# Optimization experiments

Measured on AMD Instinct MI355X. Metric: run time of the kernel, lower is better.

## Reference

```python
import math
import jax, jax.numpy as jnp
import numpy as np

C = 256          # channels
HID = 64         # max(int(C*0.25),16)
RH = 64          # max(C//4,32) router hidden
N, S, H, W = 8, 64, 16, 16
LOW_FREQ_RATIO = 0.2
ROUTER_TEMP = 1.0
LN_EPS = 1e-5

def gelu(v):
    return jax.nn.gelu(v, approximate=False)

def bn1d(v, s, b):  # folded eval-mode BatchNorm1d: (N,C,S)
    return v * s[None, :, None] + b[None, :, None]

def conv1x1(v, w, b=None):  # v:(N,Cin,S), w:(Cout,Cin)
    o = jnp.einsum('oc,ncs->nos', w, v)
    if b is not None:
        o = o + b[None, :, None]
    return o

def convk(v, w):  # v:(N,Cin,S), w:(Cout,Cin,K), 'same' padding
    k = w.shape[-1]
    return jax.lax.conv_general_dilated(v, w, (1,), [(k // 2, k // 2)],
                                        dimension_numbers=('NCH', 'OIH', 'NCH'))

def setup_inputs():
    key = jax.random.key(0)
    ks = iter(jax.random.split(key, 64))
    def nrm(shape, sc=0.02):
        return jax.random.normal(next(ks), shape, jnp.float32) * sc
    d = {}
    d['x'] = jax.random.normal(next(ks), (N, C, S, H, W), jnp.float32)
    d['ln_g'] = jnp.ones((C,), jnp.float32)
    d['ln_b'] = jnp.zeros((C,), jnp.float32)
    for k in (3, 5, 7):
        d['mb_w%d' % k] = nrm((C, 3 * C, k))
        d['mb_s%d' % k] = 1.0 + nrm((C,))
        d['mb_b%d' % k] = nrm((C,))
    d['mf_w'] = nrm((C, C)); d['mf_s'] = 1.0 + nrm((C,)); d['mf_b'] = nrm((C,))
    d['pg_w1'] = nrm((HID, 3)); d['pg_s1'] = 1.0 + nrm((HID,)); d['pg_b1'] = nrm((HID,))
    d['pg_w2'] = nrm((C, HID)); d['pg_b2'] = nrm((C,))
    d['pp_w'] = nrm((C, C)); d['pp_s'] = 1.0 + nrm((C,)); d['pp_b'] = nrm((C,))
    d['mg_w'] = nrm((C, 2 * C)); d['mg_b'] = nrm((C,))
    d['mo_w1'] = nrm((C, 3 * C)); d['mo_s1'] = 1.0 + nrm((C,)); d['mo_b1'] = nrm((C,))
    d['mo_w2'] = nrm((C, C))
    d['rt_w1'] = nrm((RH, C + 5)); d['rt_b1'] = nrm((RH,))
    d['rt_w2'] = nrm((3, RH)); d['rt_b2'] = nrm((3,))
    d['bp_w1'] = nrm((C, 4 * C)); d['bp_s1'] = 1.0 + nrm((C,)); d['bp_b1'] = nrm((C,))
    d['bp_w2'] = nrm((C, C))
    d['res_scale'] = jnp.full((1, C, 1), 0.05, jnp.float32)
    d['fg_w'] = nrm((C, C)); d['fg_b'] = nrm((C,))
    d['sg_w'] = nrm((C, C)); d['sg_s'] = 1.0 + nrm((C,)); d['sg_b'] = nrm((C,))
    return d

def _forward(x, ln_g, ln_b, mb_w3, mb_s3, mb_b3, mb_w5, mb_s5, mb_b5,
             mb_w7, mb_s7, mb_b7, mf_w, mf_s, mf_b,
             pg_w1, pg_s1, pg_b1, pg_w2, pg_b2, pp_w, pp_s, pp_b,
             mg_w, mg_b, mo_w1, mo_s1, mo_b1, mo_w2,
             rt_w1, rt_b1, rt_w2, rt_b2, bp_w1, bp_s1, bp_b1, bp_w2,
             res_scale, fg_w, fg_b, sg_w, sg_s, sg_b):
    n, c, s = x.shape[:3]
    x32 = x.astype(jnp.float32)
    desc = x32.mean(axis=(-1, -2))                     # (N,C,S)
    t = desc.transpose(0, 2, 1)                        # (N,S,C)
    mu = t.mean(-1, keepdims=True)
    var = t.var(-1, keepdims=True)
    dn = (((t - mu) / jnp.sqrt(var + LN_EPS)) * ln_g + ln_b).transpose(0, 2, 1)  # (N,C,S)

    def tdiff(v, order):
        dd = v[:, :, order:] - v[:, :, :-order]
        return jnp.pad(dd, ((0, 0), (0, 0), (order, 0)))
    diff1 = tdiff(dn, 1)
    diff2 = tdiff(dn, 2)

    # motion branch (multi-kernel conv1d + BN + GELU)
    mi = jnp.concatenate([dn, diff1, diff2], axis=1)   # (N,3C,S)
    motion = 0.0
    for w, bs, bb in ((mb_w3, mb_s3, mb_b3), (mb_w5, mb_s5, mb_b5), (mb_w7, mb_s7, mb_b7)):
        motion = motion + gelu(bn1d(convk(mi, w), bs, bb))
    motion = gelu(bn1d(conv1x1(motion / 3.0, mf_w), mf_s, mf_b))

    # FFT-based cycle / phase estimation
    tokens = dn.transpose(0, 2, 1)                     # (N,S,C)
    freq = jnp.fft.rfft(tokens, axis=1, norm='ortho')  # (N,F,C) complex
    fe = jnp.abs(freq).mean(-1)                        # (N,F)
    Fb = fe.shape[1]
    low = min(max(int(round(Fb * LOW_FREQ_RATIO)), 1), Fb - 1)
    he = fe[:, low:]
    peak_rel = jnp.argmax(he, axis=-1)                 # (N,)
    peak_idx = peak_rel + low
    peak_val = jnp.take_along_axis(he, peak_rel[:, None], axis=1)
    cycle_conf = peak_val / jnp.maximum(he.sum(axis=1, keepdims=True), 1e-6)  # (N,1)
    peak_norm = peak_idx.astype(jnp.float32)[:, None] / float(Fb - 1)
    mean_freq = freq.mean(-1)                          # (N,F) complex
    dom = jnp.take_along_axis(mean_freq, peak_idx[:, None], axis=1)[:, 0]
    dom_phase = jnp.arctan2(dom.imag, dom.real)
    tax = jnp.arange(s, dtype=jnp.float32)
    ang = (2.0 * math.pi / max(s, 1)) * peak_idx.astype(jnp.float32)
    arg = ang[:, None] * tax[None, :] + dom_phase[:, None]
    phase_cos = jnp.cos(arg)[:, None, :]               # (N,1,S)
    phase_sin = jnp.sin(arg)[:, None, :]

    cycle_token = jnp.broadcast_to(cycle_conf[:, :, None], (n, 1, s))
    pf = jnp.concatenate([phase_cos, phase_sin, cycle_token], axis=1)  # (N,3,S)
    pgate = jax.nn.sigmoid(conv1x1(gelu(bn1d(conv1x1(pf, pg_w1), pg_s1, pg_b1)), pg_w2, pg_b2))
    phase = gelu(bn1d(conv1x1(dn * pgate, pp_w), pp_s, pp_b))

    # bidirectional EMA memory via lax.scan
    gate = jax.nn.sigmoid(conv1x1(jnp.concatenate([dn, jnp.abs(diff1)], axis=1), mg_w, mg_b))
    g = gate.transpose(2, 0, 1)                        # (S,N,C)
    dd = dn.transpose(2, 0, 1)
    def step(st, gd):
        gt, dt = gd
        st = gt * st + (1.0 - gt) * dt
        return st, st
    _, fo = jax.lax.scan(step, dd[0], (g[1:], dd[1:]))
    fwd_mem = jnp.concatenate([dd[:1], fo], axis=0).transpose(1, 2, 0)
    _, bo = jax.lax.scan(step, dd[-1], (g[-2::-1], dd[-2::-1]))
    bwd_mem = jnp.concatenate([dd[-1:], bo], axis=0)[::-1].transpose(1, 2, 0)
    memory = conv1x1(gelu(bn1d(conv1x1(
        jnp.concatenate([dn, fwd_mem, bwd_mem], axis=1), mo_w1), mo_s1, mo_b1)), mo_w2)

    # router
    seq_std = dn.std(axis=2).mean(axis=1, keepdims=True)
    diff_energy = jnp.abs(diff1).mean(axis=(1, 2))[:, None]
    motion_energy = jnp.abs(motion).mean(axis=(1, 2))[:, None]
    memory_energy = jnp.abs(memory - dn).mean(axis=(1, 2))[:, None]
    stats = jnp.concatenate([seq_std, diff_energy, cycle_conf, peak_norm,
                             memory_energy + motion_energy], axis=-1)
    ri = jnp.concatenate([dn.mean(-1), stats], axis=-1)  # (N,C+5)
    hdn = gelu(ri @ rt_w1.T + rt_b1)
    logits = hdn @ rt_w2.T + rt_b2
    bw = jax.nn.softmax(logits / max(ROUTER_TEMP, 1e-6), axis=-1)  # (N,3)
    fused = (bw[:, 0, None, None] * motion + bw[:, 1, None, None] * phase
             + bw[:, 2, None, None] * memory)

    delta = conv1x1(gelu(bn1d(conv1x1(
        jnp.concatenate([dn, fused, motion - phase, memory - dn], axis=1),
        bp_w1), bp_s1, bp_b1)), bp_w2)
    delta = delta * jax.nn.sigmoid(conv1x1(dn, fg_w, fg_b))
    delta = res_scale * delta
    delta = delta[:, :, :, None, None]                 # (N,C,S,1,1)

    sp = x32.mean(axis=2)                              # (N,C,H,W)
    sg_lin = jnp.einsum('oc,nchw->nohw', sg_w, sp)
    sgate = jax.nn.sigmoid(sg_lin * sg_s[None, :, None, None] + sg_b[None, :, None, None])
    delta = delta * sgate[:, :, None, :, :]            # (N,C,S,H,W)
    return x + delta.astype(x.dtype)

def reference(x, ln_g, ln_b, mb_w3, mb_s3, mb_b3, mb_w5, mb_s5, mb_b5,
              mb_w7, mb_s7, mb_b7, mf_w, mf_s, mf_b,
              pg_w1, pg_s1, pg_b1, pg_w2, pg_b2, pp_w, pp_s, pp_b,
              mg_w, mg_b, mo_w1, mo_s1, mo_b1, mo_w2,
              rt_w1, rt_b1, rt_w2, rt_b2, bp_w1, bp_s1, bp_b1, bp_w2,
              res_scale, fg_w, fg_b, sg_w, sg_s, sg_b):
    return _forward(x, ln_g, ln_b, mb_w3, mb_s3, mb_b3, mb_w5, mb_s5, mb_b5,
                    mb_w7, mb_s7, mb_b7, mf_w, mf_s, mf_b,
                    pg_w1, pg_s1, pg_b1, pg_w2, pg_b2, pp_w, pp_s, pp_b,
                    mg_w, mg_b, mo_w1, mo_s1, mo_b1, mo_w2,
                    rt_w1, rt_b1, rt_w2, rt_b2, bp_w1, bp_s1, bp_b1, bp_w2,
                    res_scale, fg_w, fg_b, sg_w, sg_s, sg_b)
```

## Files before the change

### kernel.cpp

```cpp
#include <hip/hip_runtime.h>
#include <math.h>

namespace {

constexpr int N_ = 8, C_ = 256, S_ = 64, HW_ = 256;
constexpr int NS = N_ * S_;
constexpr int NHW = N_ * HW_;

constexpr size_t O_DESC  = 0;
constexpr size_t O_DN    = 131072;
constexpr size_t O_MOT   = 393216;
constexpr size_t O_GATE  = 524288;
constexpr size_t O_MEM   = 786432;
constexpr size_t O_PHASE = 1048576;
constexpr size_t O_DELTA = 1441792;
constexpr size_t O_SCN   = 1572864;
constexpr size_t O_SPT   = 2752512;
constexpr size_t O_SGATE = 3276800;
constexpr size_t O_FE    = 3801088;
constexpr size_t O_MFRE  = 3801600;
constexpr size_t O_MFIM  = 3802112;
constexpr size_t O_BW    = 3802656;
constexpr size_t O_ATMF  = 3802688;
constexpr size_t O_ATMG  = 3868224;
constexpr size_t O_ATMO1 = 3999296;
constexpr size_t O_ATMO2 = 4195904;
constexpr size_t O_ATPP  = 4261440;
constexpr size_t O_ATBP1 = 4326976;
constexpr size_t O_ATBP2 = 4589120;
constexpr size_t O_ATFG  = 4654656;
constexpr size_t O_ATSG  = 4720192;
constexpr size_t O_WFRAG = 4785728;
constexpr size_t O_IM2   = 6850112;
constexpr size_t O_CONVC = 8226368;

typedef __attribute__((ext_vector_type(4))) float f32x4;
typedef __attribute__((ext_vector_type(8))) short s16x8;
typedef __attribute__((ext_vector_type(8))) unsigned short u16x8;

__device__ __forceinline__ float gelu_f(float v) {
  return 0.5f * v * (1.0f + erff(v * 0.70710678118654752f));
}
__device__ __forceinline__ float sigmoid_f(float v) {
  return 1.0f / (1.0f + expf(-v));
}
__device__ __forceinline__ unsigned short f2bf(float f) {
  unsigned int u = __float_as_uint(f);
  u += 0x7fffu + ((u >> 16) & 1u);
  return (unsigned short)(u >> 16);
}

__device__ __forceinline__ float block_sum256(float v, float* scratch) {
  #pragma unroll
  for (int off = 32; off; off >>= 1) v += __shfl_down(v, off, 64);
  int w = threadIdx.x >> 6;
  __syncthreads();
  if ((threadIdx.x & 63) == 0) scratch[w] = v;
  __syncthreads();
  return scratch[0] + scratch[1] + scratch[2] + scratch[3];
}

__device__ __forceinline__ void compute_pk(
    int n, const float* __restrict__ fe, const float* __restrict__ mfre,
    const float* __restrict__ mfim,
    float& conf, float& pnorm, float& dph, float& ang) {
  const float* f = fe + n * 33;
  float best = f[7]; int bidx = 0; float hs = 0.f;
  #pragma unroll
  for (int i = 0; i < 26; ++i) {
    float v = f[7 + i];
    hs += v;
    if (v > best) { best = v; bidx = i; }
  }
  int pi = bidx + 7;
  conf = best / fmaxf(hs, 1e-6f);
  pnorm = (float)pi * (1.f / 32.f);
  dph = atan2f(mfim[n * 33 + pi], mfre[n * 33 + pi]);
  ang = (6.283185307179586f / 64.f) * (float)pi;
}

__global__ __launch_bounds__(256) void weights_kernel(
    const float* __restrict__ wmf, const float* __restrict__ wmg,
    const float* __restrict__ wmo1, const float* __restrict__ wmo2,
    const float* __restrict__ wpp, const float* __restrict__ wbp1,
    const float* __restrict__ wbp2, const float* __restrict__ wfg,
    const float* __restrict__ wsg, float* __restrict__ ws,
    const float* __restrict__ w3, const float* __restrict__ w5,
    const float* __restrict__ w7, unsigned short* __restrict__ wf) {
  int bid = blockIdx.x;
  if (bid < 960) {
    __shared__ float tile[32][33];
    int xt = bid % 120, yt = bid / 120;
    const float* src; float* dst; int K;
    if      (xt < 8)   { src = wmf;  dst = ws + O_ATMF;  K = 256;  }
    else if (xt < 24)  { src = wmg;  dst = ws + O_ATMG;  K = 512;  xt -= 8;  }
    else if (xt < 48)  { src = wmo1; dst = ws + O_ATMO1; K = 768;  xt -= 24; }
    else if (xt < 56)  { src = wmo2; dst = ws + O_ATMO2; K = 256;  xt -= 48; }
    else if (xt < 64)  { src = wpp;  dst = ws + O_ATPP;  K = 256;  xt -= 56; }
    else if (xt < 96)  { src = wbp1; dst = ws + O_ATBP1; K = 1024; xt -= 64; }
    else if (xt < 104) { src = wbp2; dst = ws + O_ATBP2; K = 256;  xt -= 96; }
    else if (xt < 112) { src = wfg;  dst = ws + O_ATFG;  K = 256;  xt -= 104;}
    else               { src = wsg;  dst = ws + O_ATSG;  K = 256;  xt -= 112;}
    int tx = threadIdx.x & 31, ty = threadIdx.x >> 5;
    int c = xt * 32 + tx;
    #pragma unroll
    for (int i = 0; i < 4; ++i) {
      int r = yt * 32 + ty + i * 8;
      tile[ty + i * 8][tx] = src[(size_t)r * K + c];
    }
    __syncthreads();
    #pragma unroll
    for (int i = 0; i < 4; ++i) {
      int cc = xt * 32 + ty + i * 8;
      dst[(size_t)cc * 256 + yt * 32 + tx] = tile[tx][ty + i * 8];
    }
  } else {
    int g = (bid - 960) * 256 + threadIdx.x;
    int lane = g & 63;
    int m16 = (g >> 6) % 48;
    int kchunk = (g >> 6) / 48;
    int o = m16 * 16 + (lane & 15);
    int conv = o >> 8, oc = o & 255;
    int q = lane >> 4;
    u16x8 outv;
    #pragma unroll
    for (int j = 0; j < 8; ++j) {
      int k = kchunk * 32 + q * 8 + j;
      int ic = k / 7;
      int tau = k - ic * 7 - 3;
      float v = 0.f;
      if (conv == 0) {
        if (tau >= -1 && tau <= 1) v = w3[((size_t)oc * 768 + ic) * 3 + (tau + 1)];
      } else if (conv == 1) {
        if (tau >= -2 && tau <= 2) v = w5[((size_t)oc * 768 + ic) * 5 + (tau + 2)];
      } else {
        v = w7[((size_t)oc * 768 + ic) * 7 + (tau + 3)];
      }
      outv[j] = f2bf(v);
    }
    *((u16x8*)wf + g) = outv;
  }
}

__global__ __launch_bounds__(256) void reduce_x_kernel(
    const float* __restrict__ x, float* __restrict__ desc_t, float* __restrict__ sp_t) {
  int nc = blockIdx.x; int n = nc >> 8; int c = nc & 255;
  int t = threadIdx.x; int w = t >> 6; int l = t & 63;
  const float4* x4 = (const float4*)x + (size_t)nc * 4096;
  float4 sa = {0.f, 0.f, 0.f, 0.f};
  for (int i = 0; i < 16; ++i) {
    int s = w * 16 + i;
    float4 v = x4[(size_t)s * 64 + l];
    sa.x += v.x; sa.y += v.y; sa.z += v.z; sa.w += v.w;
    float ds = v.x + v.y + v.z + v.w;
    #pragma unroll
    for (int off = 32; off; off >>= 1) ds += __shfl_down(ds, off, 64);
    if (l == 0) desc_t[((size_t)n * 64 + s) * 256 + c] = ds * (1.f / 256.f);
  }
  __shared__ float4 lsp[4][64];
  lsp[w][l] = sa;
  __syncthreads();
  if (t < 64) {
    float4 a = lsp[0][t], b = lsp[1][t], c2 = lsp[2][t], d = lsp[3][t];
    float4 tot;
    tot.x = a.x + b.x + c2.x + d.x; tot.y = a.y + b.y + c2.y + d.y;
    tot.z = a.z + b.z + c2.z + d.z; tot.w = a.w + b.w + c2.w + d.w;
    size_t base = ((size_t)n * 256 + t * 4) * 256 + c;
    sp_t[base]       = tot.x * (1.f / 64.f);
    sp_t[base + 256] = tot.y * (1.f / 64.f);
    sp_t[base + 512] = tot.z * (1.f / 64.f);
    sp_t[base + 768] = tot.w * (1.f / 64.f);
  }
}

__global__ __launch_bounds__(256) void ln_kernel(
    const float* __restrict__ desc_t, const float* __restrict__ g,
    const float* __restrict__ b, float* __restrict__ dn_t) {
  __shared__ float sc[4];
  int col = blockIdx.x; int t = threadIdx.x;
  float v = desc_t[(size_t)col * 256 + t];
  float s1 = block_sum256(v, sc);
  float s2 = block_sum256(v * v, sc);
  float mu = s1 * (1.f / 256.f);
  float var = s2 * (1.f / 256.f) - mu * mu;
  float r = rsqrtf(var + 1e-5f);
  dn_t[(size_t)col * 256 + t] = (v - mu) * r * g[t] + b[t];
}

__global__ __launch_bounds__(256) void post_ln_kernel(
    const float* __restrict__ dn_t, const float* __restrict__ At_mg,
    const float* __restrict__ mg_b, float* __restrict__ gate_t,
    unsigned short* __restrict__ imf,
    float* __restrict__ fe, float* __restrict__ mfre, float* __restrict__ mfim) {
  __shared__ __align__(16) float smem[2048];
  int bid = blockIdx.x;
  int t = threadIdx.x;
  if (bid < 128) {
    int c0 = bid * 4;
    float4 f0, f1;
    {
      float d[4], a[4];
      #pragma unroll
      for (int i = 0; i < 4; ++i) {
        int col = c0 + i; int s = col & 63;
        float dd = dn_t[(size_t)col * 256 + t];
        float d1 = (s >= 1) ? dd - dn_t[(size_t)(col - 1) * 256 + t] : 0.f;
        d[i] = dd; a[i] = fabsf(d1);
      }
      f0.x = d[0]; f0.y = d[1]; f0.z = d[2]; f0.w = d[3];
      f1.x = a[0]; f1.y = a[1]; f1.z = a[2]; f1.w = a[3];
    }
    *(float4*)&smem[t * 4] = f0;
    *(float4*)&smem[(256 + t) * 4] = f1;
    __syncthreads();
    float a0 = 0.f, a1 = 0.f, a2 = 0.f, a3 = 0.f;
    #pragma unroll 4
    for (int k = 0; k < 512; ++k) {
      float a = At_mg[(size_t)k * 256 + t];
      float4 b = *(const float4*)&smem[k * 4];
      a0 += a * b.x; a1 += a * b.y; a2 += a * b.z; a3 += a * b.w;
    }
    float bb = mg_b[t];
    gate_t[(size_t)(c0 + 0) * 256 + t] = sigmoid_f(a0 + bb);
    gate_t[(size_t)(c0 + 1) * 256 + t] = sigmoid_f(a1 + bb);
    gate_t[(size_t)(c0 + 2) * 256 + t] = sigmoid_f(a2 + bb);
    gate_t[(size_t)(c0 + 3) * 256 + t] = sigmoid_f(a3 + bb);
  } else if (bid < 1472) {
    int g = (bid - 128) * 256 + t;
    int lane = g & 63;
    int c16 = (g >> 6) % 32;
    int kchunk = (g >> 6) / 32;
    int col = c16 * 16 + (lane & 15);
    int n = col >> 6, s = col & 63;
    int q = lane >> 4;
    const float* base = dn_t + (size_t)n * 16384;
    u16x8 outv;
    #pragma unroll
    for (int j = 0; j < 8; ++j) {
      int k = kchunk * 32 + q * 8 + j;
      int ic = k / 7;
      int tau = k - ic * 7 - 3;
      int stream = ic >> 8, c = ic & 255;
      int sp = s + tau;
      float v = 0.f;
      if (sp >= 0 && sp < 64) {
        float d = base[(size_t)sp * 256 + c];
        if (stream == 0) v = d;
        else if (stream == 1) v = (sp >= 1) ? d - base[(size_t)(sp - 1) * 256 + c] : 0.f;
        else v = (sp >= 2) ? d - base[(size_t)(sp - 2) * 256 + c] : 0.f;
      }
      outv[j] = f2bf(v);
    }
    *((u16x8*)imf + g) = outv;
  } else {
    int b = bid - 1472; int n = b / 33; int f = b % 33;
    float* cs = smem; float* sn = smem + 64; float* scr = smem + 128;
    if (t < 64) {
      int ft = (f * t) & 63;
      float ang = -6.283185307179586f * (float)ft * (1.f / 64.f);
      cs[t] = cosf(ang); sn[t] = sinf(ang);
    }
    __syncthreads();
    float re = 0.f, im = 0.f;
    const float* base = dn_t + (size_t)n * 16384 + t;
    for (int s = 0; s < 64; ++s) {
      float v = base[(size_t)s * 256];
      re += v * cs[s]; im += v * sn[s];
    }
    re *= 0.125f; im *= 0.125f;
    float mag = sqrtf(re * re + im * im);
    float sm = block_sum256(mag, scr);
    float sr = block_sum256(re, scr);
    float si = block_sum256(im, scr);
    if (t == 0) {
      fe[b]   = sm * (1.f / 256.f);
      mfre[b] = sr * (1.f / 256.f);
      mfim[b] = si * (1.f / 256.f);
    }
  }
}

__global__ __launch_bounds__(256) void conv_scan_kernel(
    const unsigned short* __restrict__ wf, const unsigned short* __restrict__ imf,
    float* __restrict__ partial,
    const float* __restrict__ dn_t, const float* __restrict__ gate_t,
    float* __restrict__ scn) {
  __shared__ float smem[16384];
  int bid = blockIdx.x;
  int t = threadIdx.x;
  if (bid < 384) {
    int mt = bid % 12; int rem = bid / 12;
    int nt = rem % 8; int kp = rem / 8;
    int lane = t & 63;
    int w = t >> 6;
    int m16 = mt * 4 + w;
    const s16x8* wfp = (const s16x8*)wf;
    const s16x8* imp = (const s16x8*)imf;
    f32x4 acc0 = {0.f,0.f,0.f,0.f}, acc1 = {0.f,0.f,0.f,0.f};
    f32x4 acc2 = {0.f,0.f,0.f,0.f}, acc3 = {0.f,0.f,0.f,0.f};
    #pragma unroll 2
    for (int cc = 0; cc < 42; ++cc) {
      int kc = kp * 42 + cc;
      s16x8 a = wfp[(size_t)(kc * 48 + m16) * 64 + lane];
      s16x8 b0 = imp[(size_t)(kc * 32 + nt * 4 + 0) * 64 + lane];
      s16x8 b1 = imp[(size_t)(kc * 32 + nt * 4 + 1) * 64 + lane];
      s16x8 b2 = imp[(size_t)(kc * 32 + nt * 4 + 2) * 64 + lane];
      s16x8 b3 = imp[(size_t)(kc * 32 + nt * 4 + 3) * 64 + lane];
      acc0 = __builtin_amdgcn_mfma_f32_16x16x32_bf16(a, b0, acc0, 0, 0, 0);
      acc1 = __builtin_amdgcn_mfma_f32_16x16x32_bf16(a, b1, acc1, 0, 0, 0);
      acc2 = __builtin_amdgcn_mfma_f32_16x16x32_bf16(a, b2, acc2, 0, 0, 0);
      acc3 = __builtin_amdgcn_mfma_f32_16x16x32_bf16(a, b3, acc3, 0, 0, 0);
    }
    int q = lane >> 4, ln = lane & 15;
    int o0 = m16 * 16 + q * 4;
    float* pb = partial + (size_t)kp * 393216;
    #pragma unroll
    for (int r = 0; r < 4; ++r) {
      size_t row = (size_t)(o0 + r) * 512;
      pb[row + (nt * 4 + 0) * 16 + ln] = acc0[r];
      pb[row + (nt * 4 + 1) * 16 + ln] = acc1[r];
      pb[row + (nt * 4 + 2) * 16 + ln] = acc2[r];
      pb[row + (nt * 4 + 3) * 16 + ln] = acc3[r];
    }
  } else {
    int idx = bid - 384;
    int n = idx >> 1, half = idx & 1;
    float* ld = smem;
    float* lg = smem + 8192;
    const float* dsrc = dn_t + (size_t)n * 16384 + half * 128;
    const float* gsrc = gate_t + (size_t)n * 16384 + half * 128;
    for (int i = t; i < 8192; i += 256) {
      int s = i >> 7, j = i & 127;
      ld[i] = dsrc[(size_t)s * 256 + j];
      lg[i] = gsrc[(size_t)s * 256 + j];
    }
    __syncthreads();
    int cl = t & 127;
    int c = half * 128 + cl;
    size_t ob = (size_t)n * 64 * 512 + c;
    if (t < 128) {
      float st = ld[cl];
      scn[ob] = st;
      for (int s = 1; s < 64; ++s) {
        float g = lg[s * 128 + cl], d = ld[s * 128 + cl];
        st = g * st + (1.f - g) * d;
        scn[ob + (size_t)s * 512] = st;
      }
    } else {
      float st = ld[63 * 128 + cl];
      scn[ob + (size_t)63 * 512 + 256] = st;
      for (int s = 62; s >= 0; --s) {
        float g = lg[s * 128 + cl], d = ld[s * 128 + cl];
        st = g * st + (1.f - g) * d;
        scn[ob + (size_t)s * 512 + 256] = st;
      }
    }
  }
}

__global__ __launch_bounds__(256) void mid_kernel(
    const float* __restrict__ P,
    const float* __restrict__ s3, const float* __restrict__ b3,
    const float* __restrict__ s5, const float* __restrict__ b5,
    const float* __restrict__ s7, const float* __restrict__ b7,
    const float* __restrict__ At_mf, const float* __restrict__ mf_s,
    const float* __restrict__ mf_b, float* __restrict__ motion_t,
    const float* __restrict__ dn_t, const float* __restrict__ scn,
    const float* __restrict__ At1, const float* __restrict__ sc1, const float* __restrict__ bi1,
    const float* __restrict__ At2, float* __restrict__ mem_t,
    const float* __restrict__ fe, const float* __restrict__ mfre, const float* __restrict__ mfim,
    const float* __restrict__ pg_w1, const float* __restrict__ pg_s1, const float* __restrict__ pg_b1,
    const float* __restrict__ pg_w2, const float* __restrict__ pg_b2,
    const float* __restrict__ At_pp, const float* __restrict__ pp_s, const float* __restrict__ pp_b,
    float* __restrict__ phase_t,
    const float* __restrict__ At_sg, const float* __restrict__ sp_t,
    const float* __restrict__ sg_s, const float* __restrict__ sg_b,
    float* __restrict__ sgate_t) {
  __shared__ __align__(16) float smem[4096];
  int bid = blockIdx.x;
  int t = threadIdx.x;
  if (bid < 128) {
    int c0 = bid * 4;
    float4 v3 = {0,0,0,0}, v5 = {0,0,0,0}, v7 = {0,0,0,0};
    #pragma unroll
    for (int kp = 0; kp < 4; ++kp) {
      const float* base = P + (size_t)kp * 393216 + c0;
      float4 x3 = *(const float4*)(base + (size_t)t * 512);
      float4 x5 = *(const float4*)(base + (size_t)(t + 256) * 512);
      float4 x7 = *(const float4*)(base + (size_t)(t + 512) * 512);
      v3.x += x3.x; v3.y += x3.y; v3.z += x3.z; v3.w += x3.w;
      v5.x += x5.x; v5.y += x5.y; v5.z += x5.z; v5.w += x5.w;
      v7.x += x7.x; v7.y += x7.y; v7.z += x7.z; v7.w += x7.w;
    }
    float s3v = s3[t], b3v = b3[t], s5v = s5[t], b5v = b5[t], s7v = s7[t], b7v = b7[t];
    float4 ms;
    ms.x = (gelu_f(v3.x*s3v+b3v) + gelu_f(v5.x*s5v+b5v) + gelu_f(v7.x*s7v+b7v)) * (1.f/3.f);
    ms.y = (gelu_f(v3.y*s3v+b3v) + gelu_f(v5.y*s5v+b5v) + gelu_f(v7.y*s7v+b7v)) * (1.f/3.f);
    ms.z = (gelu_f(v3.z*s3v+b3v) + gelu_f(v5.z*s5v+b5v) + gelu_f(v7.z*s7v+b7v)) * (1.f/3.f);
    ms.w = (gelu_f(v3.w*s3v+b3v) + gelu_f(v5.w*s5v+b5v) + gelu_f(v7.w*s7v+b7v)) * (1.f/3.f);
    *(float4*)&smem[t * 4] = ms;
    __syncthreads();
    float a0 = 0.f, a1 = 0.f, a2 = 0.f, a3 = 0.f;
    #pragma unroll 4
    for (int k = 0; k < 256; ++k) {
      float a = At_mf[(size_t)k * 256 + t];
      float4 b = *(const float4*)&smem[k * 4];
      a0 += a * b.x; a1 += a * b.y; a2 += a * b.z; a3 += a * b.w;
    }
    float sv = mf_s[t], bv2 = mf_b[t];
    motion_t[(size_t)(c0 + 0) * 256 + t] = gelu_f(a0 * sv + bv2);
    motion_t[(size_t)(c0 + 1) * 256 + t] = gelu_f(a1 * sv + bv2);
    motion_t[(size_t)(c0 + 2) * 256 + t] = gelu_f(a2 * sv + bv2);
    motion_t[(size_t)(c0 + 3) * 256 + t] = gelu_f(a3 * sv + bv2);
  } else if (bid < 256) {
    int c0 = (bid - 128) * 4;
    float* bv = smem;
    float* h4 = smem + 3072;
    float4 r0, r1, r2;
    #pragma unroll
    for (int i = 0; i < 4; ++i) {
      int col = c0 + i;
      ((float*)&r0)[i] = dn_t[(size_t)col * 256 + t];
      ((float*)&r1)[i] = scn[(size_t)col * 512 + t];
      ((float*)&r2)[i] = scn[(size_t)col * 512 + 256 + t];
    }
    *(float4*)&bv[t * 4] = r0;
    *(float4*)&bv[(256 + t) * 4] = r1;
    *(float4*)&bv[(512 + t) * 4] = r2;
    __syncthreads();
    float a0 = 0.f, a1 = 0.f, a2 = 0.f, a3 = 0.f;
    #pragma unroll 4
    for (int k = 0; k < 768; ++k) {
      float a = At1[(size_t)k * 256 + t];
      float4 b = *(const float4*)&bv[k * 4];
      a0 += a * b.x; a1 += a * b.y; a2 += a * b.z; a3 += a * b.w;
    }
    float sv = sc1[t], bb = bi1[t];
    float4 h;
    h.x = gelu_f(a0 * sv + bb); h.y = gelu_f(a1 * sv + bb);
    h.z = gelu_f(a2 * sv + bb); h.w = gelu_f(a3 * sv + bb);
    *(float4*)&h4[t * 4] = h;
    __syncthreads();
    float c0a = 0.f, c1a = 0.f, c2a = 0.f, c3a = 0.f;
    #pragma unroll 4
    for (int k = 0; k < 256; ++k) {
      float a = At2[(size_t)k * 256 + t];
      float4 b = *(const float4*)&h4[k * 4];
      c0a += a * b.x; c1a += a * b.y; c2a += a * b.z; c3a += a * b.w;
    }
    mem_t[(size_t)(c0 + 0) * 256 + t] = c0a;
    mem_t[(size_t)(c0 + 1) * 256 + t] = c1a;
    mem_t[(size_t)(c0 + 2) * 256 + t] = c2a;
    mem_t[(size_t)(c0 + 3) * 256 + t] = c3a;
  } else if (bid < 384) {
    int c0 = (bid - 256) * 4; int n = c0 >> 6; int s0 = c0 & 63;
    float* hh4 = smem;
    float* pin4 = smem + 256;
    float conf, pnorm, dph, ang;
    compute_pk(n, fe, mfre, mfim, conf, pnorm, dph, ang);
    (void)pnorm;
    if (t < 64) {
      float w0 = pg_w1[t * 3 + 0], w1 = pg_w1[t * 3 + 1], w2 = pg_w1[t * 3 + 2];
      float sv = pg_s1[t], bb = pg_b1[t];
      float4 hv;
      #pragma unroll
      for (int i = 0; i < 4; ++i) {
        float arg = ang * (float)(s0 + i) + dph;
        float v = w0 * cosf(arg) + w1 * sinf(arg) + w2 * conf;
        ((float*)&hv)[i] = gelu_f(v * sv + bb);
      }
      *(float4*)&hh4[t * 4] = hv;
    }
    __syncthreads();
    float p0, p1, p2, p3;
    {
      float bb = pg_b2[t];
      float a0 = bb, a1 = bb, a2 = bb, a3 = bb;
      const float* wrow = pg_w2 + t * 64;
      #pragma unroll 8
      for (int j = 0; j < 64; ++j) {
        float w = wrow[j];
        float4 h = *(const float4*)&hh4[j * 4];
        a0 += w * h.x; a1 += w * h.y; a2 += w * h.z; a3 += w * h.w;
      }
      p0 = sigmoid_f(a0); p1 = sigmoid_f(a1); p2 = sigmoid_f(a2); p3 = sigmoid_f(a3);
    }
    float4 pin;
    pin.x = dn_t[(size_t)(c0 + 0) * 256 + t] * p0;
    pin.y = dn_t[(size_t)(c0 + 1) * 256 + t] * p1;
    pin.z = dn_t[(size_t)(c0 + 2) * 256 + t] * p2;
    pin.w = dn_t[(size_t)(c0 + 3) * 256 + t] * p3;
    *(float4*)&pin4[t * 4] = pin;
    __syncthreads();
    float a0 = 0.f, a1 = 0.f, a2 = 0.f, a3 = 0.f;
    #pragma unroll 4
    for (int k = 0; k < 256; ++k) {
      float a = At_pp[(size_t)k * 256 + t];
      float4 b = *(const float4*)&pin4[k * 4];
      a0 += a * b.x; a1 += a * b.y; a2 += a * b.z; a3 += a * b.w;
    }
    float sv = pp_s[t], bb = pp_b[t];
    phase_t[(size_t)(c0 + 0) * 256 + t] = gelu_f(a0 * sv + bb);
    phase_t[(size_t)(c0 + 1) * 256 + t] = gelu_f(a1 * sv + bb);
    phase_t[(size_t)(c0 + 2) * 256 + t] = gelu_f(a2 * sv + bb);
    phase_t[(size_t)(c0 + 3) * 256 + t] = gelu_f(a3 * sv + bb);
  } else {
    int c0 = (bid - 384) * 4;
    float4 r0;
    #pragma unroll
    for (int i = 0; i < 4; ++i) {
      ((float*)&r0)[i] = sp_t[(size_t)(c0 + i) * 256 + t];
    }
    *(float4*)&smem[t * 4] = r0;
    __syncthreads();
    float a0 = 0.f, a1 = 0.f, a2 = 0.f, a3 = 0.f;
    #pragma unroll 4
    for (int k = 0; k < 256; ++k) {
      float a = At_sg[(size_t)k * 256 + t];
      float4 b = *(const float4*)&smem[k * 4];
      a0 += a * b.x; a1 += a * b.y; a2 += a * b.z; a3 += a * b.w;
    }
    float sv = sg_s[t], bb = sg_b[t];
    sgate_t[(size_t)(c0 + 0) * 256 + t] = sigmoid_f(a0 * sv + bb);
    sgate_t[(size_t)(c0 + 1) * 256 + t] = sigmoid_f(a1 * sv + bb);
    sgate_t[(size_t)(c0 + 2) * 256 + t] = sigmoid_f(a2 * sv + bb);
    sgate_t[(size_t)(c0 + 3) * 256 + t] = sigmoid_f(a3 * sv + bb);
  }
}

__global__ __launch_bounds__(256) void router_kernel(
    const float* __restrict__ dn_t, const float* __restrict__ motion_t,
    const float* __restrict__ memory_t,
    const float* __restrict__ fe, const float* __restrict__ mfre,
    const float* __restrict__ mfim,
    const float* __restrict__ rt_w1, const float* __restrict__ rt_b1,
    const float* __restrict__ rt_w2, const float* __restrict__ rt_b2,
    float* __restrict__ bw) {
  int n = blockIdx.x; int c = threadIdx.x;
  __shared__ float ri[261];
  __shared__ float h2[64];
  __shared__ float lg[3];
  __shared__ float sc[4];
  float sum = 0.f, sq = 0.f, ad1 = 0.f, amot = 0.f, amem = 0.f, prev = 0.f;
  for (int s = 0; s < 64; ++s) {
    size_t i = ((size_t)n * 64 + s) * 256 + c;
    float d = dn_t[i];
    sum += d; sq += d * d;
    if (s > 0) ad1 += fabsf(d - prev);
    prev = d;
    amot += fabsf(motion_t[i]);
    amem += fabsf(memory_t[i] - d);
  }
  float mean = sum * (1.f / 64.f);
  float var = sq * (1.f / 64.f) - mean * mean;
  float stdc = sqrtf(fmaxf(var, 0.f));
  ri[c] = mean;
  float rstd = block_sum256(stdc, sc);
  float rad1 = block_sum256(ad1, sc);
  float rmot = block_sum256(amot, sc);
  float rmem = block_sum256(amem, sc);
  if (c == 0) {
    float conf, pnorm, dph, ang;
    compute_pk(n, fe, mfre, mfim, conf, pnorm, dph, ang);
    (void)dph; (void)ang;
    ri[256] = rstd * (1.f / 256.f);
    ri[257] = rad1 * (1.f / 16384.f);
    ri[258] = conf;
    ri[259] = pnorm;
    ri[260] = (rmem + rmot) * (1.f / 16384.f);
  }
  __syncthreads();
  if (c < 64) {
    float acc = rt_b1[c];
    const float* wrow = rt_w1 + c * 261;
    for (int i = 0; i < 261; ++i) acc += wrow[i] * ri[i];
    h2[c] = gelu_f(acc);
  }
  __syncthreads();
  if (c < 3) {
    float acc = rt_b2[c];
    const float* wrow = rt_w2 + c * 64;
    #pragma unroll 8
    for (int j = 0; j < 64; ++j) acc += wrow[j] * h2[j];
    lg[c] = acc;
  }
  __syncthreads();
  if (c == 0) {
    float m = fmaxf(lg[0], fmaxf(lg[1], lg[2]));
    float e0 = expf(lg[0] - m), e1 = expf(lg[1] - m), e2 = expf(lg[2] - m);
    float inv = 1.f / (e0 + e1 + e2);
    bw[n * 3 + 0] = e0 * inv; bw[n * 3 + 1] = e1 * inv; bw[n * 3 + 2] = e2 * inv;
  }
}

__global__ __launch_bounds__(256) void delta_kernel(
    const float* __restrict__ dn_t, const float* __restrict__ motion_t,
    const float* __restrict__ phase_t, const float* __restrict__ mem_t,
    const float* __restrict__ bw,
    const float* __restrict__ At_fg, const float* __restrict__ fg_b,
    const float* __restrict__ At1, const float* __restrict__ sc1, const float* __restrict__ bi1,
    const float* __restrict__ At2, const float* __restrict__ rs,
    float* __restrict__ delta_t) {
  __shared__ __align__(16) float bv[1024];
  __shared__ __align__(16) float4 part[4][64];
  __shared__ float hs[256];
  __shared__ float fgs[256];
  int col = blockIdx.x; int n = col >> 6; int t = threadIdx.x;
  int w = t >> 6, ln = t & 63;
  int oq = t >> 2, oc = t & 3;
  float w0 = bw[n * 3 + 0], w1 = bw[n * 3 + 1], w2 = bw[n * 3 + 2];
  size_t idx = (size_t)col * 256 + t;
  float d = dn_t[idx], m = motion_t[idx], p = phase_t[idx], me = mem_t[idx];
  bv[t]       = d;
  bv[256 + t] = w0 * m + w1 * p + w2 * me;
  bv[512 + t] = m - p;
  bv[768 + t] = me - d;
  __syncthreads();
  {
    float a0 = 0.f, a1 = 0.f, a2 = 0.f, a3 = 0.f;
    int k0 = w * 64;
    #pragma unroll 4
    for (int k = k0; k < k0 + 64; ++k) {
      float b = bv[k];
      float4 a = *(const float4*)(At_fg + (size_t)k * 256 + ln * 4);
      a0 += a.x * b; a1 += a.y * b; a2 += a.z * b; a3 += a.w * b;
    }
    float4 pr; pr.x = a0; pr.y = a1; pr.z = a2; pr.w = a3;
    part[w][ln] = pr;
  }
  __syncthreads();
  {
    float r = ((const float*)&part[0][oq])[oc] + ((const float*)&part[1][oq])[oc]
            + ((const float*)&part[2][oq])[oc] + ((const float*)&part[3][oq])[oc];
    fgs[t] = sigmoid_f(r + fg_b[t]);
  }
  __syncthreads();
  {
    float a0 = 0.f, a1 = 0.f, a2 = 0.f, a3 = 0.f;
    int k0 = w * 256;
    #pragma unroll 4
    for (int k = k0; k < k0 + 256; ++k) {
      float b = bv[k];
      float4 a = *(const float4*)(At1 + (size_t)k * 256 + ln * 4);
      a0 += a.x * b; a1 += a.y * b; a2 += a.z * b; a3 += a.w * b;
    }
    float4 pr; pr.x = a0; pr.y = a1; pr.z = a2; pr.w = a3;
    part[w][ln] = pr;
  }
  __syncthreads();
  {
    float r = ((const float*)&part[0][oq])[oc] + ((const float*)&part[1][oq])[oc]
            + ((const float*)&part[2][oq])[oc] + ((const float*)&part[3][oq])[oc];
    hs[t] = gelu_f(r * sc1[t] + bi1[t]);
  }
  __syncthreads();
  {
    float a0 = 0.f, a1 = 0.f, a2 = 0.f, a3 = 0.f;
    int k0 = w * 64;
    #pragma unroll 4
    for (int k = k0; k < k0 + 64; ++k) {
      float b = hs[k];
      float4 a = *(const float4*)(At2 + (size_t)k * 256 + ln * 4);
      a0 += a.x * b; a1 += a.y * b; a2 += a.z * b; a3 += a.w * b;
    }
    float4 pr; pr.x = a0; pr.y = a1; pr.z = a2; pr.w = a3;
    part[w][ln] = pr;
  }
  __syncthreads();
  {
    float r = ((const float*)&part[0][oq])[oc] + ((const float*)&part[1][oq])[oc]
            + ((const float*)&part[2][oq])[oc] + ((const float*)&part[3][oq])[oc];
    delta_t[idx] = r * fgs[t] * rs[t];
  }
}

__global__ __launch_bounds__(256) void final_kernel(
    const float* __restrict__ x, const float* __restrict__ delta_t,
    const float* __restrict__ sgate_t, float* __restrict__ out) {
  int nc = blockIdx.x; int n = nc >> 8; int c = nc & 255;
  int t = threadIdx.x;
  __shared__ float dlt[64];
  __shared__ float4 sgs4[64];
  if (t < 64) dlt[t] = delta_t[((size_t)n * 64 + t) * 256 + c];
  ((float*)sgs4)[t] = sgate_t[((size_t)n * 256 + t) * 256 + c];
  __syncthreads();
  const float4* x4 = (const float4*)x + (size_t)nc * 4096;
  float4* o4 = (float4*)out + (size_t)nc * 4096;
  int w = t >> 6, l = t & 63;
  float4 sg = sgs4[l];
  for (int i = 0; i < 16; ++i) {
    int s = w * 16 + i;
    float d = dlt[s];
    float4 v = x4[(size_t)s * 64 + l];
    v.x += d * sg.x; v.y += d * sg.y; v.z += d * sg.z; v.w += d * sg.w;
    o4[(size_t)s * 64 + l] = v;
  }
}

}

extern "C" void kernel_launch(void* const* d_in, const int* in_sizes, int n_in,
                              void* d_out, int out_size, void* d_ws, size_t ws_size,
                              hipStream_t stream) {
  const float* x      = (const float*)d_in[0];
  const float* ln_g   = (const float*)d_in[1];
  const float* ln_b   = (const float*)d_in[2];
  const float* mb_w3  = (const float*)d_in[3];
  const float* mb_s3  = (const float*)d_in[4];
  const float* mb_b3  = (const float*)d_in[5];
  const float* mb_w5  = (const float*)d_in[6];
  const float* mb_s5  = (const float*)d_in[7];
  const float* mb_b5  = (const float*)d_in[8];
  const float* mb_w7  = (const float*)d_in[9];
  const float* mb_s7  = (const float*)d_in[10];
  const float* mb_b7  = (const float*)d_in[11];
  const float* mf_w   = (const float*)d_in[12];
  const float* mf_s   = (const float*)d_in[13];
  const float* mf_b   = (const float*)d_in[14];
  const float* pg_w1  = (const float*)d_in[15];
  const float* pg_s1  = (const float*)d_in[16];
  const float* pg_b1  = (const float*)d_in[17];
  const float* pg_w2  = (const float*)d_in[18];
  const float* pg_b2  = (const float*)d_in[19];
  const float* pp_w   = (const float*)d_in[20];
  const float* pp_s   = (const float*)d_in[21];
  const float* pp_b   = (const float*)d_in[22];
  const float* mg_w   = (const float*)d_in[23];
  const float* mg_b   = (const float*)d_in[24];
  const float* mo_w1  = (const float*)d_in[25];
  const float* mo_s1  = (const float*)d_in[26];
  const float* mo_b1  = (const float*)d_in[27];
  const float* mo_w2  = (const float*)d_in[28];
  const float* rt_w1  = (const float*)d_in[29];
  const float* rt_b1  = (const float*)d_in[30];
  const float* rt_w2  = (const float*)d_in[31];
  const float* rt_b2  = (const float*)d_in[32];
  const float* bp_w1  = (const float*)d_in[33];
  const float* bp_s1  = (const float*)d_in[34];
  const float* bp_b1  = (const float*)d_in[35];
  const float* bp_w2  = (const float*)d_in[36];
  const float* res_sc = (const float*)d_in[37];
  const float* fg_w   = (const float*)d_in[38];
  const float* fg_b   = (const float*)d_in[39];
  const float* sg_w   = (const float*)d_in[40];
  const float* sg_s   = (const float*)d_in[41];
  const float* sg_b   = (const float*)d_in[42];
  float* ws = (float*)d_ws;
  float* out = (float*)d_out;
  unsigned short* wfrag = (unsigned short*)(ws + O_WFRAG);
  unsigned short* im2   = (unsigned short*)(ws + O_IM2);

  weights_kernel<<<2976, 256, 0, stream>>>(mf_w, mg_w, mo_w1, mo_w2, pp_w, bp_w1,
      bp_w2, fg_w, sg_w, ws, mb_w3, mb_w5, mb_w7, wfrag);
  reduce_x_kernel<<<2048, 256, 0, stream>>>(x, ws + O_DESC, ws + O_SPT);
  ln_kernel<<<512, 256, 0, stream>>>(ws + O_DESC, ln_g, ln_b, ws + O_DN);
  post_ln_kernel<<<1736, 256, 0, stream>>>(ws + O_DN, ws + O_ATMG, mg_b, ws + O_GATE,
      im2, ws + O_FE, ws + O_MFRE, ws + O_MFIM);
  conv_scan_kernel<<<400, 256, 0, stream>>>(wfrag, im2, ws + O_CONVC,
      ws + O_DN, ws + O_GATE, ws + O_SCN);
  mid_kernel<<<896, 256, 0, stream>>>(ws + O_CONVC, mb_s3, mb_b3, mb_s5, mb_b5,
      mb_s7, mb_b7, ws + O_ATMF, mf_s, mf_b, ws + O_MOT,
      ws + O_DN, ws + O_SCN, ws + O_ATMO1, mo_s1, mo_b1, ws + O_ATMO2, ws + O_MEM,
      ws + O_FE, ws + O_MFRE, ws + O_MFIM,
      pg_w1, pg_s1, pg_b1, pg_w2, pg_b2, ws + O_ATPP, pp_s, pp_b, ws + O_PHASE,
      ws + O_ATSG, ws + O_SPT, sg_s, sg_b, ws + O_SGATE);
  router_kernel<<<8, 256, 0, stream>>>(ws + O_DN, ws + O_MOT, ws + O_MEM,
      ws + O_FE, ws + O_MFRE, ws + O_MFIM, rt_w1, rt_b1, rt_w2, rt_b2, ws + O_BW);
  delta_kernel<<<512, 256, 0, stream>>>(ws + O_DN, ws + O_MOT, ws + O_PHASE, ws + O_MEM,
      ws + O_BW, ws + O_ATFG, fg_b, ws + O_ATBP1, bp_s1, bp_b1, ws + O_ATBP2, res_sc,
      ws + O_DELTA);
  final_kernel<<<2048, 256, 0, stream>>>(x, ws + O_DELTA, ws + O_SGATE, out);
}
```

Before: 564.4 us.

## Merge weight prep with x reduction, fuse spatial gate into final kernel

Combines the weight-transpose/fragment kernel and the x reduction kernel into one launch, removing a launch and letting the two independent workloads overlap. The spatial gate GEMV moves out of mid_kernel into final_kernel, where each block computes its own 256 sigmoid gates from sp_t and a sg_w row, so the sgate intermediate buffer is gone. The bidirectional scan now uses 4 blocks per batch instead of 2 for more parallelism. The cost is extra per-block GEMV work in final_kernel, which repeats reads of sp_t across channels.

```diff
diff --git a/kernel.cpp b/kernel.cpp
--- a/kernel.cpp
+++ b/kernel.cpp
@@ -16,7 +16,6 @@
 constexpr size_t O_DELTA = 1441792;
 constexpr size_t O_SCN   = 1572864;
 constexpr size_t O_SPT   = 2752512;
-constexpr size_t O_SGATE = 3276800;
 constexpr size_t O_FE    = 3801088;
 constexpr size_t O_MFRE  = 3801600;
 constexpr size_t O_MFIM  = 3802112;
@@ -29,7 +28,6 @@
 constexpr size_t O_ATBP1 = 4326976;
 constexpr size_t O_ATBP2 = 4589120;
 constexpr size_t O_ATFG  = 4654656;
-constexpr size_t O_ATSG  = 4720192;
 constexpr size_t O_WFRAG = 4785728;
 constexpr size_t O_IM2   = 6850112;
 constexpr size_t O_CONVC = 8226368;
@@ -79,18 +77,49 @@
   ang = (6.283185307179586f / 64.f) * (float)pi;
 }
 
-__global__ __launch_bounds__(256) void weights_kernel(
+__global__ __launch_bounds__(256) void reduce_weights_kernel(
+    const float* __restrict__ x, float* __restrict__ desc_t, float* __restrict__ sp_t,
     const float* __restrict__ wmf, const float* __restrict__ wmg,
     const float* __restrict__ wmo1, const float* __restrict__ wmo2,
     const float* __restrict__ wpp, const float* __restrict__ wbp1,
     const float* __restrict__ wbp2, const float* __restrict__ wfg,
-    const float* __restrict__ wsg, float* __restrict__ ws,
+    float* __restrict__ ws,
     const float* __restrict__ w3, const float* __restrict__ w5,
     const float* __restrict__ w7, unsigned short* __restrict__ wf) {
   int bid = blockIdx.x;
-  if (bid < 960) {
+  int t = threadIdx.x;
+  if (bid < 2048) {
+    int nc = bid; int n = nc >> 8; int c = nc & 255;
+    int w = t >> 6; int l = t & 63;
+    const float4* x4 = (const float4*)x + (size_t)nc * 4096;
+    float4 sa = {0.f, 0.f, 0.f, 0.f};
+    for (int i = 0; i < 16; ++i) {
+      int s = w * 16 + i;
+      float4 v = x4[(size_t)s * 64 + l];
+      sa.x += v.x; sa.y += v.y; sa.z += v.z; sa.w += v.w;
+      float ds = v.x + v.y + v.z + v.w;
+      #pragma unroll
+      for (int off = 32; off; off >>= 1) ds += __shfl_down(ds, off, 64);
+      if (l == 0) desc_t[((size_t)n * 64 + s) * 256 + c] = ds * (1.f / 256.f);
+    }
+    __shared__ float4 lsp[4][64];
+    lsp[w][l] = sa;
+    __syncthreads();
+    if (t < 64) {
+      float4 a = lsp[0][t], b = lsp[1][t], c2 = lsp[2][t], d = lsp[3][t];
+      float4 tot;
+      tot.x = a.x + b.x + c2.x + d.x; tot.y = a.y + b.y + c2.y + d.y;
+      tot.z = a.z + b.z + c2.z + d.z; tot.w = a.w + b.w + c2.w + d.w;
+      size_t base = ((size_t)n * 256 + t * 4) * 256 + c;
+      sp_t[base]       = tot.x * (1.f / 64.f);
+      sp_t[base + 256] = tot.y * (1.f / 64.f);
+      sp_t[base + 512] = tot.z * (1.f / 64.f);
+      sp_t[base + 768] = tot.w * (1.f / 64.f);
+    }
+  } else if (bid < 2048 + 896) {
     __shared__ float tile[32][33];
-    int xt = bid % 120, yt = bid / 120;
+    int b2 = bid - 2048;
+    int xt = b2 % 112, yt = b2 / 112;
     const float* src; float* dst; int K;
     if      (xt < 8)   { src = wmf;  dst = ws + O_ATMF;  K = 256;  }
     else if (xt < 24)  { src = wmg;  dst = ws + O_ATMG;  K = 512;  xt -= 8;  }
@@ -99,9 +128,8 @@
     else if (xt < 64)  { src = wpp;  dst = ws + O_ATPP;  K = 256;  xt -= 56; }
     else if (xt < 96)  { src = wbp1; dst = ws + O_ATBP1; K = 1024; xt -= 64; }
     else if (xt < 104) { src = wbp2; dst = ws + O_ATBP2; K = 256;  xt -= 96; }
-    else if (xt < 112) { src = wfg;  dst = ws + O_ATFG;  K = 256;  xt -= 104;}
-    else               { src = wsg;  dst = ws + O_ATSG;  K = 256;  xt -= 112;}
-    int tx = threadIdx.x & 31, ty = threadIdx.x >> 5;
+    else               { src = wfg;  dst = ws + O_ATFG;  K = 256;  xt -= 104;}
+    int tx = t & 31, ty = t >> 5;
     int c = xt * 32 + tx;
     #pragma unroll
     for (int i = 0; i < 4; ++i) {
@@ -115,7 +143,7 @@
       dst[(size_t)cc * 256 + yt * 32 + tx] = tile[tx][ty + i * 8];
     }
   } else {
-    int g = (bid - 960) * 256 + threadIdx.x;
+    int g = (bid - 2048 - 896) * 256 + t;
     int lane = g & 63;
     int m16 = (g >> 6) % 48;
     int kchunk = (g >> 6) / 48;
@@ -139,37 +167,6 @@
       outv[j] = f2bf(v);
     }
     *((u16x8*)wf + g) = outv;
-  }
-}
-
-__global__ __launch_bounds__(256) void reduce_x_kernel(
-    const float* __restrict__ x, float* __restrict__ desc_t, float* __restrict__ sp_t) {
-  int nc = blockIdx.x; int n = nc >> 8; int c = nc & 255;
-  int t = threadIdx.x; int w = t >> 6; int l = t & 63;
-  const float4* x4 = (const float4*)x + (size_t)nc * 4096;
-  float4 sa = {0.f, 0.f, 0.f, 0.f};
-  for (int i = 0; i < 16; ++i) {
-    int s = w * 16 + i;
-    float4 v = x4[(size_t)s * 64 + l];
-    sa.x += v.x; sa.y += v.y; sa.z += v.z; sa.w += v.w;
-    float ds = v.x + v.y + v.z + v.w;
-    #pragma unroll
-    for (int off = 32; off; off >>= 1) ds += __shfl_down(ds, off, 64);
-    if (l == 0) desc_t[((size_t)n * 64 + s) * 256 + c] = ds * (1.f / 256.f);
-  }
-  __shared__ float4 lsp[4][64];
-  lsp[w][l] = sa;
-  __syncthreads();
-  if (t < 64) {
-    float4 a = lsp[0][t], b = lsp[1][t], c2 = lsp[2][t], d = lsp[3][t];
-    float4 tot;
-    tot.x = a.x + b.x + c2.x + d.x; tot.y = a.y + b.y + c2.y + d.y;
-    tot.z = a.z + b.z + c2.z + d.z; tot.w = a.w + b.w + c2.w + d.w;
-    size_t base = ((size_t)n * 256 + t * 4) * 256 + c;
-    sp_t[base]       = tot.x * (1.f / 64.f);
-    sp_t[base + 256] = tot.y * (1.f / 64.f);
-    sp_t[base + 512] = tot.z * (1.f / 64.f);
-    sp_t[base + 768] = tot.w * (1.f / 64.f);
   }
 }
 
@@ -285,7 +282,7 @@
     float* __restrict__ partial,
     const float* __restrict__ dn_t, const float* __restrict__ gate_t,
     float* __restrict__ scn) {
-  __shared__ float smem[16384];
+  __shared__ float smem[8192];
   int bid = blockIdx.x;
   int t = threadIdx.x;
   if (bid < 384) {
@@ -324,33 +321,33 @@
     }
   } else {
     int idx = bid - 384;
-    int n = idx >> 1, half = idx & 1;
+    int n = idx >> 2, qr = idx & 3;
     float* ld = smem;
-    float* lg = smem + 8192;
-    const float* dsrc = dn_t + (size_t)n * 16384 + half * 128;
-    const float* gsrc = gate_t + (size_t)n * 16384 + half * 128;
-    for (int i = t; i < 8192; i += 256) {
-      int s = i >> 7, j = i & 127;
+    float* lg = smem + 4096;
+    const float* dsrc = dn_t + (size_t)n * 16384 + qr * 64;
+    const float* gsrc = gate_t + (size_t)n * 16384 + qr * 64;
+    for (int i = t; i < 4096; i += 256) {
+      int s = i >> 6, j = i & 63;
       ld[i] = dsrc[(size_t)s * 256 + j];
       lg[i] = gsrc[(size_t)s * 256 + j];
     }
     __syncthreads();
-    int cl = t & 127;
-    int c = half * 128 + cl;
+    int cl = t & 63;
+    int c = qr * 64 + cl;
     size_t ob = (size_t)n * 64 * 512 + c;
-    if (t < 128) {
+    if (t < 64) {
       float st = ld[cl];
       scn[ob] = st;
       for (int s = 1; s < 64; ++s) {
-        float g = lg[s * 128 + cl], d = ld[s * 128 + cl];
+        float g = lg[s * 64 + cl], d = ld[s * 64 + cl];
         st = g * st + (1.f - g) * d;
         scn[ob + (size_t)s * 512] = st;
       }
-    } else {
-      float st = ld[63 * 128 + cl];
+    } else if (t < 128) {
+      float st = ld[63 * 64 + cl];
       scn[ob + (size_t)63 * 512 + 256] = st;
       for (int s = 62; s >= 0; --s) {
-        float g = lg[s * 128 + cl], d = ld[s * 128 + cl];
+        float g = lg[s * 64 + cl], d = ld[s * 64 + cl];
         st = g * st + (1.f - g) * d;
         scn[ob + (size_t)s * 512 + 256] = st;
       }
@@ -372,10 +369,7 @@
     const float* __restrict__ pg_w1, const float* __restrict__ pg_s1, const float* __restrict__ pg_b1,
     const float* __restrict__ pg_w2, const float* __restrict__ pg_b2,
     const float* __restrict__ At_pp, const float* __restrict__ pp_s, const float* __restrict__ pp_b,
-    float* __restrict__ phase_t,
-    const float* __restrict__ At_sg, const float* __restrict__ sp_t,
-    const float* __restrict__ sg_s, const float* __restrict__ sg_b,
-    float* __restrict__ sgate_t) {
+    float* __restrict__ phase_t) {
   __shared__ __align__(16) float smem[4096];
   int bid = blockIdx.x;
   int t = threadIdx.x;
@@ -452,7 +446,7 @@
     mem_t[(size_t)(c0 + 1) * 256 + t] = c1a;
     mem_t[(size_t)(c0 + 2) * 256 + t] = c2a;
     mem_t[(size_t)(c0 + 3) * 256 + t] = c3a;
-  } else if (bid < 384) {
+  } else {
     int c0 = (bid - 256) * 4; int n = c0 >> 6; int s0 = c0 & 63;
     float* hh4 = smem;
     float* pin4 = smem + 256;
@@ -504,27 +498,6 @@
     phase_t[(size_t)(c0 + 1) * 256 + t] = gelu_f(a1 * sv + bb);
     phase_t[(size_t)(c0 + 2) * 256 + t] = gelu_f(a2 * sv + bb);
     phase_t[(size_t)(c0 + 3) * 256 + t] = gelu_f(a3 * sv + bb);
-  } else {
-    int c0 = (bid - 384) * 4;
-    float4 r0;
-    #pragma unroll
-    for (int i = 0; i < 4; ++i) {
-      ((float*)&r0)[i] = sp_t[(size_t)(c0 + i) * 256 + t];
-    }
-    *(float4*)&smem[t * 4] = r0;
-    __syncthreads();
-    float a0 = 0.f, a1 = 0.f, a2 = 0.f, a3 = 0.f;
-    #pragma unroll 4
-    for (int k = 0; k < 256; ++k) {
-      float a = At_sg[(size_t)k * 256 + t];
-      float4 b = *(const float4*)&smem[k * 4];
-      a0 += a * b.x; a1 += a * b.y; a2 += a * b.z; a3 += a * b.w;
-    }
-    float sv = sg_s[t], bb = sg_b[t];
-    sgate_t[(size_t)(c0 + 0) * 256 + t] = sigmoid_f(a0 * sv + bb);
-    sgate_t[(size_t)(c0 + 1) * 256 + t] = sigmoid_f(a1 * sv + bb);
-    sgate_t[(size_t)(c0 + 2) * 256 + t] = sigmoid_f(a2 * sv + bb);
-    sgate_t[(size_t)(c0 + 3) * 256 + t] = sigmoid_f(a3 * sv + bb);
   }
 }
 
@@ -676,18 +649,34 @@
 
 __global__ __launch_bounds__(256) void final_kernel(
     const float* __restrict__ x, const float* __restrict__ delta_t,
-    const float* __restrict__ sgate_t, float* __restrict__ out) {
+    const float* __restrict__ sp_t, const float* __restrict__ sg_w,
+    const float* __restrict__ sg_s, const float* __restrict__ sg_b,
+    float* __restrict__ out) {
   int nc = blockIdx.x; int n = nc >> 8; int c = nc & 255;
   int t = threadIdx.x;
   __shared__ float dlt[64];
-  __shared__ float4 sgs4[64];
+  __shared__ float wcol[256];
+  __shared__ __align__(16) float sgl[256];
   if (t < 64) dlt[t] = delta_t[((size_t)n * 64 + t) * 256 + c];
-  ((float*)sgs4)[t] = sgate_t[((size_t)n * 256 + t) * 256 + c];
+  wcol[t] = sg_w[(size_t)c * 256 + t];
+  __syncthreads();
+  {
+    const float* sprow = sp_t + ((size_t)n * 256 + t) * 256;
+    float acc = 0.f;
+    for (int k = 0; k < 256; k += 4) {
+      float4 s4 = *(const float4*)(sprow + k);
+      acc += wcol[k + 0] * s4.x;
+      acc += wcol[k + 1] * s4.y;
+      acc += wcol[k + 2] * s4.z;
+      acc += wcol[k + 3] * s4.w;
+    }
+    sgl[t] = sigmoid_f(acc * sg_s[c] + sg_b[c]);
+  }
   __syncthreads();
   const float4* x4 = (const float4*)x + (size_t)nc * 4096;
   float4* o4 = (float4*)out + (size_t)nc * 4096;
   int w = t >> 6, l = t & 63;
-  float4 sg = sgs4[l];
+  float4 sg = *(const float4*)&sgl[l * 4];
   for (int i = 0; i < 16; ++i) {
     int s = w * 16 + i;
     float d = dlt[s];
@@ -750,24 +739,24 @@
   unsigned short* wfrag = (unsigned short*)(ws + O_WFRAG);
   unsigned short* im2   = (unsigned short*)(ws + O_IM2);
 
-  weights_kernel<<<2976, 256, 0, stream>>>(mf_w, mg_w, mo_w1, mo_w2, pp_w, bp_w1,
-      bp_w2, fg_w, sg_w, ws, mb_w3, mb_w5, mb_w7, wfrag);
-  reduce_x_kernel<<<2048, 256, 0, stream>>>(x, ws + O_DESC, ws + O_SPT);
+  reduce_weights_kernel<<<4960, 256, 0, stream>>>(x, ws + O_DESC, ws + O_SPT,
+      mf_w, mg_w, mo_w1, mo_w2, pp_w, bp_w1, bp_w2, fg_w, ws,
+      mb_w3, mb_w5, mb_w7, wfrag);
   ln_kernel<<<512, 256, 0, stream>>>(ws + O_DESC, ln_g, ln_b, ws + O_DN);
   post_ln_kernel<<<1736, 256, 0, stream>>>(ws + O_DN, ws + O_ATMG, mg_b, ws + O_GATE,
       im2, ws + O_FE, ws + O_MFRE, ws + O_MFIM);
-  conv_scan_kernel<<<400, 256, 0, stream>>>(wfrag, im2, ws + O_CONVC,
+  conv_scan_kernel<<<416, 256, 0, stream>>>(wfrag, im2, ws + O_CONVC,
       ws + O_DN, ws + O_GATE, ws + O_SCN);
-  mid_kernel<<<896, 256, 0, stream>>>(ws + O_CONVC, mb_s3, mb_b3, mb_s5, mb_b5,
+  mid_kernel<<<384, 256, 0, stream>>>(ws + O_CONVC, mb_s3, mb_b3, mb_s5, mb_b5,
       mb_s7, mb_b7, ws + O_ATMF, mf_s, mf_b, ws + O_MOT,
       ws + O_DN, ws + O_SCN, ws + O_ATMO1, mo_s1, mo_b1, ws + O_ATMO2, ws + O_MEM,
       ws + O_FE, ws + O_MFRE, ws + O_MFIM,
-      pg_w1, pg_s1, pg_b1, pg_w2, pg_b2, ws + O_ATPP, pp_s, pp_b, ws + O_PHASE,
-      ws + O_ATSG, ws + O_SPT, sg_s, sg_b, ws + O_SGATE);
+      pg_w1, pg_s1, pg_b1, pg_w2, pg_b2, ws + O_ATPP, pp_s, pp_b, ws + O_PHASE);
   router_kernel<<<8, 256, 0, stream>>>(ws + O_DN, ws + O_MOT, ws + O_MEM,
       ws + O_FE, ws + O_MFRE, ws + O_MFIM, rt_w1, rt_b1, rt_w2, rt_b2, ws + O_BW);
   delta_kernel<<<512, 256, 0, stream>>>(ws + O_DN, ws + O_MOT, ws + O_PHASE, ws + O_MEM,
       ws + O_BW, ws + O_ATFG, fg_b, ws + O_ATBP1, bp_s1, bp_b1, ws + O_ATBP2, res_sc,
       ws + O_DELTA);
-  final_kernel<<<2048, 256, 0, stream>>>(x, ws + O_DELTA, ws + O_SGATE, out);
-}
+  final_kernel<<<2048, 256, 0, stream>>>(x, ws + O_DELTA, ws + O_SPT,
+      sg_w, sg_s, sg_b, out);
+}
```

Measured after the change: 598.5 us. 6.0% more time.
